# Optimization experiments

Measured on AMD Instinct MI355X. Metric: run time of the kernel, lower is better.

Reference implementation:

```python
import jax, jax.numpy as jnp
import numpy as np

NEG_BIG = -1e30  # stand-in for -inf in the log-space eps state


def wkv_scan(w, u, k, v, alpha0, beta0, eps0):
    """Numerically-stable RWKV WKV recurrence.

    w: exp(time_decay) (D,), u: time_first (D,)
    k, v: (B, T, D); alpha0, beta0, eps0: (B, D)
    Returns wkv (B, T, D) and final state.
    """
    def step(carry, kv_t):
        alpha, beta, eps = carry
        kt, vt = kv_t  # (B, D)
        # output: (e^{u+k} v + alpha) / (e^{u+k} + beta), stabilized
        ww = u + kt
        tau = jnp.maximum(eps, ww)
        e1 = jnp.exp(eps - tau)
        e2 = jnp.exp(ww - tau)
        out = (e1 * alpha + e2 * vt) / (e1 * beta + e2)
        # state update with decay: alpha' = e^{-w} alpha + e^{k} v (log-space)
        ww2 = eps - w
        tau2 = jnp.maximum(ww2, kt)
        e1b = jnp.exp(ww2 - tau2)
        e2b = jnp.exp(kt - tau2)
        return (e1b * alpha + e2b * vt, e1b * beta + e2b, tau2), out

    kT = jnp.swapaxes(k, 0, 1)  # (T, B, D)
    vT = jnp.swapaxes(v, 0, 1)
    (_, _, _), outs = jax.lax.scan(step, (alpha0, beta0, eps0), (kT, vT))
    return jnp.swapaxes(outs, 0, 1)  # (B, T, D)


def setup_inputs() -> dict:
    key = jax.random.key(0)
    ks = jax.random.split(key, 10)
    B, T, D = 4, 2048, 2048
    scale = 1.0 / np.sqrt(D)
    x = jax.random.normal(ks[0], (B, T, D), dtype=jnp.float32)
    time_decay = jax.random.uniform(ks[1], (D,), minval=-1.0, maxval=1.0)
    time_first = 0.1 * jax.random.normal(ks[2], (D,))
    time_mix_k = jax.random.uniform(ks[3], (1, 1, D))
    time_mix_v = jax.random.uniform(ks[4], (1, 1, D))
    time_mix_r = jax.random.uniform(ks[5], (1, 1, D))
    Wk = scale * jax.random.normal(ks[6], (D, D))
    Wv = scale * jax.random.normal(ks[7], (D, D))
    Wr = scale * jax.random.normal(ks[8], (D, D))
    Wo = scale * jax.random.normal(ks[9], (D, D))
    return {"x": x, "time_decay": time_decay, "time_first": time_first,
            "time_mix_k": time_mix_k, "time_mix_v": time_mix_v,
            "time_mix_r": time_mix_r, "Wk": Wk, "Wv": Wv, "Wr": Wr, "Wo": Wo}


def reference(x, time_decay, time_first, time_mix_k, time_mix_v, time_mix_r,
              Wk, Wv, Wr, Wo):
    B, T, D = x.shape
    # time_shift: prepend zero init_x, drop last token
    last_x = jnp.concatenate([jnp.zeros((B, 1, D), x.dtype), x[:, :-1, :]], axis=1)
    k = jnp.einsum('btd,ed->bte', x * time_mix_k + last_x * (1 - time_mix_k), Wk)
    v = jnp.einsum('btd,ed->bte', x * time_mix_v + last_x * (1 - time_mix_v), Wv)
    r = jnp.einsum('btd,ed->bte', x * time_mix_r + last_x * (1 - time_mix_r), Wr)
    sr = jax.nn.sigmoid(r)
    w = jnp.exp(time_decay)
    alpha0 = jnp.zeros((B, D), x.dtype)
    beta0 = jnp.zeros((B, D), x.dtype)
    eps0 = jnp.full((B, D), NEG_BIG, x.dtype)
    wkv = wkv_scan(w, time_first, k, v, alpha0, beta0, eps0)
    return jnp.einsum('btd,ed->bte', wkv * sr, Wo)
```

## Files before the change

### kernel.cpp

```cpp
#include <hip/hip_runtime.h>
#include <stdint.h>

typedef __bf16 bf16x8 __attribute__((ext_vector_type(8)));
typedef float f32x4 __attribute__((ext_vector_type(4)));

#define BM 128
#define BN 128
#define BK 64

__global__ void prep_kernel(const float* __restrict__ w0, const float* __restrict__ w1,
                            const float* __restrict__ w2, const float* __restrict__ w3,
                            __bf16* __restrict__ o0, __bf16* __restrict__ o1,
                            __bf16* __restrict__ o2, __bf16* __restrict__ o3,
                            long DD, unsigned cvtBlocks,
                            const float* __restrict__ x,
                            const float* __restrict__ mk, const float* __restrict__ mv,
                            const float* __restrict__ mr,
                            __bf16* __restrict__ ok, __bf16* __restrict__ ov,
                            __bf16* __restrict__ orr,
                            int T, int D, long total) {
    if (blockIdx.x < cvtBlocks) {
        long idx = ((long)blockIdx.x * blockDim.x + threadIdx.x) * 8;
        if (idx >= 4 * DD) return;
        int w = (int)(idx / DD);
        long off = idx - (long)w * DD;
        const float* in = (w == 0) ? w0 : (w == 1) ? w1 : (w == 2) ? w2 : w3;
        __bf16* out     = (w == 0) ? o0 : (w == 1) ? o1 : (w == 2) ? o2 : o3;
        f32x4 a = *(const f32x4*)(in + off);
        f32x4 b = *(const f32x4*)(in + off + 4);
        bf16x8 o;
#pragma unroll
        for (int i = 0; i < 4; ++i) { o[i] = (__bf16)a[i]; o[i + 4] = (__bf16)b[i]; }
        *(bf16x8*)(out + off) = o;
    } else {
        long idx = ((long)(blockIdx.x - cvtBlocks) * blockDim.x + threadIdx.x) * 8;
        if (idx >= total) return;
        int d = (int)(idx % D);
        long bt = idx / D;
        int t = (int)(bt % T);

        f32x4 x0 = *(const f32x4*)(x + idx);
        f32x4 x1 = *(const f32x4*)(x + idx + 4);
        f32x4 l0 = {}, l1 = {};
        if (t != 0) {
            l0 = *(const f32x4*)(x + idx - D);
            l1 = *(const f32x4*)(x + idx - D + 4);
        }
        const float* mw[3] = {mk, mv, mr};
        __bf16* ow[3] = {ok, ov, orr};
#pragma unroll
        for (int s = 0; s < 3; ++s) {
            f32x4 m0 = *(const f32x4*)(mw[s] + d);
            f32x4 m1 = *(const f32x4*)(mw[s] + d + 4);
            bf16x8 o;
#pragma unroll
            for (int i = 0; i < 4; ++i) {
                o[i]     = (__bf16)(x0[i] * m0[i] + l0[i] * (1.0f - m0[i]));
                o[i + 4] = (__bf16)(x1[i] * m1[i] + l1[i] * (1.0f - m1[i]));
            }
            *(bf16x8*)(ow[s] + idx) = o;
        }
    }
}

template <typename CT>
__device__ __attribute__((always_inline))
void gemm_body(const __bf16* __restrict__ A, const __bf16* __restrict__ Bt,
               CT* __restrict__ C, int M, int N, int K) {
    __shared__ __align__(16) __bf16 sA[BM * BK];
    __shared__ __align__(16) __bf16 sB[BN * BK];

    const int tid  = threadIdx.x;
    const int lane = tid & 63;
    const int wave = tid >> 6;

    const int id  = blockIdx.y * gridDim.x + blockIdx.x;
    const int nwg = gridDim.x * gridDim.y;
    const int wg  = (id & 7) * (nwg >> 3) + (id >> 3);
    const int bx  = wg % gridDim.x;
    const int by  = wg / gridDim.x;
    const int m0 = by * BM;
    const int n0 = bx * BN;

    const int wm = (wave & 1) * 64;
    const int wn = (wave >> 1) * 64;

    const int l8 = lane >> 3;
    const int c8 = lane & 7;
    const int cg = c8 ^ l8;

    const int q  = lane >> 4;
    const int ml = lane & 15;

    f32x4 acc[4][4] = {};

    for (int k0 = 0; k0 < K; k0 += BK) {
#pragma unroll
        for (int i = 0; i < 4; ++i) {
            const int cl  = wave * 4 + i;
            const int row = cl * 8 + l8;
            const __bf16* gA = A  + (long)(m0 + row) * K + (k0 + cg * 8);
            const __bf16* gB = Bt + (long)(n0 + row) * K + (k0 + cg * 8);
            __builtin_amdgcn_global_load_lds(
                (const __attribute__((address_space(1))) void*)gA,
                (__attribute__((address_space(3))) void*)(sA + cl * 512), 16, 0, 0);
            __builtin_amdgcn_global_load_lds(
                (const __attribute__((address_space(1))) void*)gB,
                (__attribute__((address_space(3))) void*)(sB + cl * 512), 16, 0, 0);
        }
        __syncthreads();

#pragma unroll
        for (int kk = 0; kk < BK; kk += 32) {
            bf16x8 af[4], bfr[4];
#pragma unroll
            for (int i = 0; i < 4; ++i) {
                int row = wm + i * 16 + ml;
                int cl  = ((kk >> 3) + q) ^ (row & 7);
                af[i] = *(const bf16x8*)(sA + row * BK + cl * 8);
            }
#pragma unroll
            for (int j = 0; j < 4; ++j) {
                int row = wn + j * 16 + ml;
                int cl  = ((kk >> 3) + q) ^ (row & 7);
                bfr[j] = *(const bf16x8*)(sB + row * BK + cl * 8);
            }
#pragma unroll
            for (int i = 0; i < 4; ++i)
#pragma unroll
                for (int j = 0; j < 4; ++j)
                    acc[i][j] = __builtin_amdgcn_mfma_f32_16x16x32_bf16(
                        af[i], bfr[j], acc[i][j], 0, 0, 0);
        }
        __syncthreads();
    }

#pragma unroll
    for (int i = 0; i < 4; ++i)
#pragma unroll
        for (int j = 0; j < 4; ++j)
#pragma unroll
            for (int rg = 0; rg < 4; ++rg) {
                int row = m0 + wm + i * 16 + q * 4 + rg;
                int col = n0 + wn + j * 16 + ml;
                C[(long)row * N + col] = (CT)acc[i][j][rg];
            }
}

template <typename CT>
__global__ __launch_bounds__(256, 3)
void gemm_bt(const __bf16* __restrict__ A, const __bf16* __restrict__ Bt,
             CT* __restrict__ C, int M, int N, int K) {
    gemm_body<CT>(A, Bt, C, M, N, K);
}

__global__ __launch_bounds__(256, 3)
void gemm_bt2(const __bf16* __restrict__ A0, const __bf16* __restrict__ A1,
              const __bf16* __restrict__ B0, const __bf16* __restrict__ B1,
              __bf16* __restrict__ C0, __bf16* __restrict__ C1,
              int M, int N, int K) {
    if (blockIdx.z == 0) gemm_body<__bf16>(A0, B0, C0, M, N, K);
    else                 gemm_body<__bf16>(A1, B1, C1, M, N, K);
}

__global__ void wkv_pass1(const float* __restrict__ kk, const __bf16* __restrict__ vv,
                          const float* __restrict__ td,
                          float* __restrict__ al, float* __restrict__ bl,
                          float* __restrict__ el,
                          int Bn, int T, int D, int C, int L) {
    int gid = blockIdx.x * blockDim.x + threadIdx.x;
    int BD = Bn * D;
    if (gid >= BD * C) return;
    int c  = gid / BD;
    int bd = gid - c * BD;
    int b  = bd / D;
    int d  = bd - b * D;

    float w = __expf(td[d]);
    float alpha = 0.f, beta = 0.f, eps = -1e30f;
    long base = ((long)b * T + (long)c * L) * D + d;

    const int P = 8;
    float kb0[P], vb0[P], kb1[P], vb1[P];

    auto step = [&](float kt, float vt) {
        float ww2  = eps - w;
        float tau2 = fmaxf(ww2, kt);
        float e1b  = __expf(ww2 - tau2);
        float e2b  = __expf(kt - tau2);
        alpha = e1b * alpha + e2b * vt;
        beta  = e1b * beta + e2b;
        eps   = tau2;
    };

#pragma unroll
    for (int j = 0; j < P; ++j) {
        long o = base + (long)j * D;
        kb0[j] = kk[o]; vb0[j] = (float)vv[o];
    }
    for (int t0 = 0; t0 < L; t0 += 2 * P) {
#pragma unroll
        for (int j = 0; j < P; ++j) {
            long o = base + (long)(t0 + P + j) * D;
            kb1[j] = kk[o]; vb1[j] = (float)vv[o];
        }
#pragma unroll
        for (int j = 0; j < P; ++j) step(kb0[j], vb0[j]);
        if (t0 + 2 * P < L) {
#pragma unroll
            for (int j = 0; j < P; ++j) {
                long o = base + (long)(t0 + 2 * P + j) * D;
                kb0[j] = kk[o]; vb0[j] = (float)vv[o];
            }
        }
#pragma unroll
        for (int j = 0; j < P; ++j) step(kb1[j], vb1[j]);
    }
    al[gid] = alpha; bl[gid] = beta; el[gid] = eps;
}

__global__ void wkv_pass2(const float* __restrict__ kk, const __bf16* __restrict__ vv,
                          const __bf16* __restrict__ rr,
                          const float* __restrict__ td, const float* __restrict__ tf,
                          const float* __restrict__ al, const float* __restrict__ bl,
                          const float* __restrict__ el,
                          __bf16* __restrict__ out,
                          int Bn, int T, int D, int C, int L) {
    int gid = blockIdx.x * blockDim.x + threadIdx.x;
    int BD = Bn * D;
    if (gid >= BD * C) return;
    int c  = gid / BD;
    int bd = gid - c * BD;
    int b  = bd / D;
    int d  = bd - b * D;

    float u = tf[d];
    float w = __expf(td[d]);

    float alpha = 0.f, beta = 0.f, eps = -1e30f;
    {
        float wL = w * (float)L;
        for (int cc = 0; cc < c; ++cc) {
            int idx = cc * BD + bd;
            float ed  = eps - wL;
            float la = al[idx], lb = bl[idx], le = el[idx];
            float tau = fmaxf(ed, le);
            float e1  = __expf(ed - tau);
            float e2  = __expf(le - tau);
            alpha = alpha * e1 + la * e2;
            beta  = beta * e1 + lb * e2;
            eps   = tau;
        }
    }

    long base = ((long)b * T + (long)c * L) * D + d;

    const int P = 8;
    float kb0[P], vb0[P], rb0[P], kb1[P], vb1[P], rb1[P];

    auto step = [&](float kt, float vt, float rt, int tIdx) {
        float ww  = u + kt;
        float tau = fmaxf(eps, ww);
        float e1  = __expf(eps - tau);
        float e2  = __expf(ww - tau);
        float num = e1 * alpha + e2 * vt;
        float den = e1 * beta + e2;
        float o_  = num * __builtin_amdgcn_rcpf(den);
        float ww2  = eps - w;
        float tau2 = fmaxf(ww2, kt);
        float e1b  = __expf(ww2 - tau2);
        float e2b  = __expf(kt - tau2);
        alpha = e1b * alpha + e2b * vt;
        beta  = e1b * beta + e2b;
        eps   = tau2;
        float sr = __builtin_amdgcn_rcpf(1.0f + __expf(-rt));
        out[base + (long)tIdx * D] = (__bf16)(o_ * sr);
    };

#pragma unroll
    for (int j = 0; j < P; ++j) {
        long o = base + (long)j * D;
        kb0[j] = kk[o]; vb0[j] = (float)vv[o]; rb0[j] = (float)rr[o];
    }
    for (int t0 = 0; t0 < L; t0 += 2 * P) {
#pragma unroll
        for (int j = 0; j < P; ++j) {
            long o = base + (long)(t0 + P + j) * D;
            kb1[j] = kk[o]; vb1[j] = (float)vv[o]; rb1[j] = (float)rr[o];
        }
#pragma unroll
        for (int j = 0; j < P; ++j) step(kb0[j], vb0[j], rb0[j], t0 + j);
        if (t0 + 2 * P < L) {
#pragma unroll
            for (int j = 0; j < P; ++j) {
                long o = base + (long)(t0 + 2 * P + j) * D;
                kb0[j] = kk[o]; vb0[j] = (float)vv[o]; rb0[j] = (float)rr[o];
            }
        }
#pragma unroll
        for (int j = 0; j < P; ++j) step(kb1[j], vb1[j], rb1[j], t0 + P + j);
    }
}

extern "C" void kernel_launch(void* const* d_in, const int* in_sizes, int n_in,
                              void* d_out, int out_size, void* d_ws, size_t ws_size,
                              hipStream_t stream) {
    const float* x  = (const float*)d_in[0];
    const float* td = (const float*)d_in[1];
    const float* tf = (const float*)d_in[2];
    const float* mk = (const float*)d_in[3];
    const float* mv = (const float*)d_in[4];
    const float* mr = (const float*)d_in[5];
    const float* Wk = (const float*)d_in[6];
    const float* Wv = (const float*)d_in[7];
    const float* Wr = (const float*)d_in[8];
    const float* Wo = (const float*)d_in[9];
    float* out = (float*)d_out;

    const int D = in_sizes[1];
    const int T = 2048;
    const long total = (long)in_sizes[0];
    const int Bn = (int)(total / ((long)T * D));
    const int M = Bn * T;
    const long DD = (long)D * D;
    const int C = 64;
    const int L = T / C;
    const int BD = Bn * D;
    const int S = BD * C;

    char* p = (char*)d_ws;
    __bf16* xmk = (__bf16*)p;            p += total * 2;
    __bf16* xmv = (__bf16*)p;            p += total * 2;
    __bf16* xmr = (__bf16*)p;            p += total * 2;
    __bf16* wkb = (__bf16*)p;            p += DD * 2;
    __bf16* wvb = (__bf16*)p;            p += DD * 2;
    __bf16* wrb = (__bf16*)p;            p += DD * 2;
    __bf16* wob = (__bf16*)p;            p += DD * 2;
    __bf16* vb  = (__bf16*)p;            p += total * 2;
    __bf16* rb  = (__bf16*)p;            p += total * 2;

    float*  kf = (float*)xmv;
    __bf16* xo = xmk;
    float*  st = (float*)wkb;
    float *al = st, *bl = st + S, *el = st + 2 * S;

    unsigned cvtBlocks = (unsigned)((4 * DD / 8 + 255) / 256);
    unsigned mixBlocks = (unsigned)((total / 8 + 255) / 256);
    dim3 prepGrid(cvtBlocks + mixBlocks);
    dim3 gemmGrid(D / BN, M / BM);
    dim3 gemm2Grid(D / BN, M / BM, 2);
    dim3 p12Grid((S + 255) / 256);

    prep_kernel<<<prepGrid, 256, 0, stream>>>(Wk, Wv, Wr, Wo, wkb, wvb, wrb, wob,
                                              DD, cvtBlocks,
                                              x, mk, mv, mr, xmk, xmv, xmr,
                                              T, D, total);

    gemm_bt2<<<gemm2Grid, 256, 0, stream>>>(xmv, xmr, wvb, wrb, vb, rb, M, D, D);
    gemm_bt<float><<<gemmGrid, 256, 0, stream>>>(xmk, wkb, kf, M, D, D);

    wkv_pass1<<<p12Grid, 256, 0, stream>>>(kf, vb, td, al, bl, el, Bn, T, D, C, L);
    wkv_pass2<<<p12Grid, 256, 0, stream>>>(kf, vb, rb, td, tf, al, bl, el, xo,
                                           Bn, T, D, C, L);

    gemm_bt<float><<<gemmGrid, 256, 0, stream>>>(xo, wob, out, M, D, D);
}
```

Baseline: 517.5 us.

## Use 256x256 triple-buffered 8-wave GEMM and fuse k/v/r projections into one launch

Replaces the 128x128 single-stage GEMM with a 256x256 tile, 512-thread kernel. It uses a three-deep LDS ring fed by global_load_lds with explicit vmcnt waits and barriers, plus s_setprio around the MFMA bursts, so global loads overlap compute and each loaded tile is reused more. The k, v and r projections now run in a single 3-slice launch, with the k output stored in the output buffer instead of the workspace. The WKV chunk count drops from 64 to 32, which changes the balance between parallelism and serial scan length. Risks include lower occupancy, more register pressure from 32 accumulators per thread, and hand-written waitcnt sequencing that must be exactly right.

```diff
diff --git a/kernel.cpp b/kernel.cpp
--- a/kernel.cpp
+++ b/kernel.cpp
@@ -3,10 +3,6 @@
 
 typedef __bf16 bf16x8 __attribute__((ext_vector_type(8)));
 typedef float f32x4 __attribute__((ext_vector_type(4)));
-
-#define BM 128
-#define BN 128
-#define BK 64
 
 __global__ void prep_kernel(const float* __restrict__ w0, const float* __restrict__ w1,
                             const float* __restrict__ w2, const float* __restrict__ w3,
@@ -66,101 +62,134 @@
 template <typename CT>
 __device__ __attribute__((always_inline))
 void gemm_body(const __bf16* __restrict__ A, const __bf16* __restrict__ Bt,
-               CT* __restrict__ C, int M, int N, int K) {
-    __shared__ __align__(16) __bf16 sA[BM * BK];
-    __shared__ __align__(16) __bf16 sB[BN * BK];
-
+               CT* __restrict__ C, int M, int N, int K,
+               __bf16* sA, __bf16* sB) {
     const int tid  = threadIdx.x;
     const int lane = tid & 63;
     const int wave = tid >> 6;
+    const int wm = wave >> 2;
+    const int wn = wave & 3;
 
     const int id  = blockIdx.y * gridDim.x + blockIdx.x;
     const int nwg = gridDim.x * gridDim.y;
     const int wg  = (id & 7) * (nwg >> 3) + (id >> 3);
     const int bx  = wg % gridDim.x;
     const int by  = wg / gridDim.x;
-    const int m0 = by * BM;
-    const int n0 = bx * BN;
-
-    const int wm = (wave & 1) * 64;
-    const int wn = (wave >> 1) * 64;
-
-    const int l8 = lane >> 3;
-    const int c8 = lane & 7;
-    const int cg = c8 ^ l8;
+    const int m0 = by * 256;
+    const int n0 = bx * 256;
+
+    const int srow = tid >> 2;
+    const int scol = ((tid & 3) ^ ((tid >> 3) & 3)) << 3;
+    const __bf16* gA0 = A  + (long)(m0 + srow) * K + scol;
+    const __bf16* gB0 = Bt + (long)(n0 + srow) * K + scol;
+    const int ldsoff = wave * 512;
+    const long rstep = (long)128 * K;
 
     const int q  = lane >> 4;
     const int ml = lane & 15;
-
-    f32x4 acc[4][4] = {};
-
-    for (int k0 = 0; k0 < K; k0 += BK) {
-#pragma unroll
-        for (int i = 0; i < 4; ++i) {
-            const int cl  = wave * 4 + i;
-            const int row = cl * 8 + l8;
-            const __bf16* gA = A  + (long)(m0 + row) * K + (k0 + cg * 8);
-            const __bf16* gB = Bt + (long)(n0 + row) * K + (k0 + cg * 8);
-            __builtin_amdgcn_global_load_lds(
-                (const __attribute__((address_space(1))) void*)gA,
-                (__attribute__((address_space(3))) void*)(sA + cl * 512), 16, 0, 0);
-            __builtin_amdgcn_global_load_lds(
-                (const __attribute__((address_space(1))) void*)gB,
-                (__attribute__((address_space(3))) void*)(sB + cl * 512), 16, 0, 0);
-        }
-        __syncthreads();
-
-#pragma unroll
-        for (int kk = 0; kk < BK; kk += 32) {
-            bf16x8 af[4], bfr[4];
-#pragma unroll
-            for (int i = 0; i < 4; ++i) {
-                int row = wm + i * 16 + ml;
-                int cl  = ((kk >> 3) + q) ^ (row & 7);
-                af[i] = *(const bf16x8*)(sA + row * BK + cl * 8);
-            }
-#pragma unroll
-            for (int j = 0; j < 4; ++j) {
-                int row = wn + j * 16 + ml;
-                int cl  = ((kk >> 3) + q) ^ (row & 7);
-                bfr[j] = *(const bf16x8*)(sB + row * BK + cl * 8);
-            }
-#pragma unroll
-            for (int i = 0; i < 4; ++i)
-#pragma unroll
-                for (int j = 0; j < 4; ++j)
-                    acc[i][j] = __builtin_amdgcn_mfma_f32_16x16x32_bf16(
-                        af[i], bfr[j], acc[i][j], 0, 0, 0);
-        }
-        __syncthreads();
-    }
-
-#pragma unroll
-    for (int i = 0; i < 4; ++i)
+    const int coff = ((q ^ (ml >> 1)) & 3) << 3;
+
+    f32x4 acc[8][4] = {};
+    bf16x8 af[4], bfr[4];
+
+    auto stage = [&](int buf, int t, int r) {
+        __builtin_amdgcn_global_load_lds(
+            (const __attribute__((address_space(1))) void*)(gA0 + r * rstep + t * 32),
+            (__attribute__((address_space(3))) void*)(sA + buf * 8192 + r * 4096 + ldsoff),
+            16, 0, 0);
+        __builtin_amdgcn_global_load_lds(
+            (const __attribute__((address_space(1))) void*)(gB0 + r * rstep + t * 32),
+            (__attribute__((address_space(3))) void*)(sB + buf * 8192 + r * 4096 + ldsoff),
+            16, 0, 0);
+    };
+
+    const int NT = K >> 5;
+
+    stage(0, 0, 0); stage(0, 0, 1);
+    stage(1, 1, 0); stage(1, 1, 1);
+    asm volatile("s_waitcnt vmcnt(4)" ::: "memory");
+    __builtin_amdgcn_s_barrier();
+
+    int b0 = 0, bs = 2;
+    for (int t = 0; t < NT; ++t) {
+        const __bf16* pa = sA + b0 * 8192 + wm * (128 * 32);
+        const __bf16* pb = sB + b0 * 8192 + wn * (64 * 32);
+        const bool st = (t + 2) < NT;
+
+#pragma unroll
+        for (int fi = 0; fi < 4; ++fi)
+            af[fi] = *(const bf16x8*)(pa + (fi * 16 + ml) * 32 + coff);
+#pragma unroll
+        for (int fj = 0; fj < 4; ++fj)
+            bfr[fj] = *(const bf16x8*)(pb + (fj * 16 + ml) * 32 + coff);
+        if (st) stage(bs, t + 2, 0);
+        __builtin_amdgcn_s_barrier();
+        asm volatile("s_waitcnt lgkmcnt(0)" ::: "memory");
+        __builtin_amdgcn_s_setprio(1);
+#pragma unroll
+        for (int fi = 0; fi < 4; ++fi)
+#pragma unroll
+            for (int fj = 0; fj < 4; ++fj)
+                acc[fi][fj] = __builtin_amdgcn_mfma_f32_16x16x32_bf16(
+                    af[fi], bfr[fj], acc[fi][fj], 0, 0, 0);
+        __builtin_amdgcn_s_setprio(0);
+        __builtin_amdgcn_s_barrier();
+
+#pragma unroll
+        for (int fi = 0; fi < 4; ++fi)
+            af[fi] = *(const bf16x8*)(pa + ((fi + 4) * 16 + ml) * 32 + coff);
+        if (st) stage(bs, t + 2, 1);
+        __builtin_amdgcn_s_barrier();
+        asm volatile("s_waitcnt lgkmcnt(0)" ::: "memory");
+        __builtin_amdgcn_s_setprio(1);
+#pragma unroll
+        for (int fi = 0; fi < 4; ++fi)
+#pragma unroll
+            for (int fj = 0; fj < 4; ++fj)
+                acc[4 + fi][fj] = __builtin_amdgcn_mfma_f32_16x16x32_bf16(
+                    af[fi], bfr[fj], acc[4 + fi][fj], 0, 0, 0);
+        __builtin_amdgcn_s_setprio(0);
+        if (st)                { asm volatile("s_waitcnt vmcnt(4)" ::: "memory"); }
+        else if (t + 1 < NT)   { asm volatile("s_waitcnt vmcnt(0)" ::: "memory"); }
+        if (t + 1 < NT) __builtin_amdgcn_s_barrier();
+
+        b0 = (b0 == 2) ? 0 : b0 + 1;
+        bs = (bs == 2) ? 0 : bs + 1;
+    }
+
+#pragma unroll
+    for (int i = 0; i < 8; ++i)
 #pragma unroll
         for (int j = 0; j < 4; ++j)
 #pragma unroll
             for (int rg = 0; rg < 4; ++rg) {
-                int row = m0 + wm + i * 16 + q * 4 + rg;
-                int col = n0 + wn + j * 16 + ml;
+                int row = m0 + wm * 128 + i * 16 + q * 4 + rg;
+                int col = n0 + wn * 64 + j * 16 + ml;
                 C[(long)row * N + col] = (CT)acc[i][j][rg];
             }
 }
 
 template <typename CT>
-__global__ __launch_bounds__(256, 3)
+__global__ __launch_bounds__(512, 2)
 void gemm_bt(const __bf16* __restrict__ A, const __bf16* __restrict__ Bt,
              CT* __restrict__ C, int M, int N, int K) {
-    gemm_body<CT>(A, Bt, C, M, N, K);
-}
-
-__global__ __launch_bounds__(256, 3)
-void gemm_bt2(const __bf16* __restrict__ A0, const __bf16* __restrict__ A1,
-              const __bf16* __restrict__ B0, const __bf16* __restrict__ B1,
-              __bf16* __restrict__ C0, __bf16* __restrict__ C1,
-              int M, int N, int K) {
-    if (blockIdx.z == 0) gemm_body<__bf16>(A0, B0, C0, M, N, K);
-    else                 gemm_body<__bf16>(A1, B1, C1, M, N, K);
+    __shared__ __align__(16) __bf16 sA[3 * 8192];
+    __shared__ __align__(16) __bf16 sB[3 * 8192];
+    gemm_body<CT>(A, Bt, C, M, N, K, sA, sB);
+}
+
+__global__ __launch_bounds__(512, 2)
+void gemm3(const __bf16* __restrict__ Av, const __bf16* __restrict__ Ar,
+           const __bf16* __restrict__ Ak,
+           const __bf16* __restrict__ Bv, const __bf16* __restrict__ Br,
+           const __bf16* __restrict__ Bk,
+           __bf16* __restrict__ Cv, __bf16* __restrict__ Cr,
+           float* __restrict__ Ck, int M, int N, int K) {
+    __shared__ __align__(16) __bf16 sA[3 * 8192];
+    __shared__ __align__(16) __bf16 sB[3 * 8192];
+    if (blockIdx.z == 0)      gemm_body<__bf16>(Av, Bv, Cv, M, N, K, sA, sB);
+    else if (blockIdx.z == 1) gemm_body<__bf16>(Ar, Br, Cr, M, N, K, sA, sB);
+    else                      gemm_body<float>(Ak, Bk, Ck, M, N, K, sA, sB);
 }
 
 __global__ void wkv_pass1(const float* __restrict__ kk, const __bf16* __restrict__ vv,
@@ -323,7 +352,7 @@
     const int Bn = (int)(total / ((long)T * D));
     const int M = Bn * T;
     const long DD = (long)D * D;
-    const int C = 64;
+    const int C = 32;
     const int L = T / C;
     const int BD = Bn * D;
     const int S = BD * C;
@@ -339,7 +368,7 @@
     __bf16* vb  = (__bf16*)p;            p += total * 2;
     __bf16* rb  = (__bf16*)p;            p += total * 2;
 
-    float*  kf = (float*)xmv;
+    float*  kf = (float*)d_out;
     __bf16* xo = xmk;
     float*  st = (float*)wkb;
     float *al = st, *bl = st + S, *el = st + 2 * S;
@@ -347,8 +376,8 @@
     unsigned cvtBlocks = (unsigned)((4 * DD / 8 + 255) / 256);
     unsigned mixBlocks = (unsigned)((total / 8 + 255) / 256);
     dim3 prepGrid(cvtBlocks + mixBlocks);
-    dim3 gemmGrid(D / BN, M / BM);
-    dim3 gemm2Grid(D / BN, M / BM, 2);
+    dim3 gemm3Grid(D / 256, M / 256, 3);
+    dim3 gemmGrid(D / 256, M / 256);
     dim3 p12Grid((S + 255) / 256);
 
     prep_kernel<<<prepGrid, 256, 0, stream>>>(Wk, Wv, Wr, Wo, wkb, wvb, wrb, wob,
@@ -356,12 +385,12 @@
                                               x, mk, mv, mr, xmk, xmv, xmr,
                                               T, D, total);
 
-    gemm_bt2<<<gemm2Grid, 256, 0, stream>>>(xmv, xmr, wvb, wrb, vb, rb, M, D, D);
-    gemm_bt<float><<<gemmGrid, 256, 0, stream>>>(xmk, wkb, kf, M, D, D);
+    gemm3<<<gemm3Grid, 512, 0, stream>>>(xmv, xmr, xmk, wvb, wrb, wkb,
+                                         vb, rb, kf, M, D, D);
 
     wkv_pass1<<<p12Grid, 256, 0, stream>>>(kf, vb, td, al, bl, el, Bn, T, D, C, L);
     wkv_pass2<<<p12Grid, 256, 0, stream>>>(kf, vb, rb, td, tf, al, bl, el, xo,
                                            Bn, T, D, C, L);
 
-    gemm_bt<float><<<gemmGrid, 256, 0, stream>>>(xo, wob, out, M, D, D);
-}
+    gemm_bt<float><<<gemmGrid, 512, 0, stream>>>(xo, wob, out, M, D, D);
+}
```

Result: no change. 518.6 us (+0.2%).
